# Optimization experiments

Hardware: AMD Instinct MI355X
Metric: run time of the kernel (lower is better)

## Reference

```python
import jax, jax.numpy as jnp
import numpy as np

N_HEAD = 16


def setup_inputs() -> dict:
    key = jax.random.key(0)
    ks = jax.random.split(key, 5)
    B, T, C = 2, 2048, 1024
    s = 1.0 / np.sqrt(C)
    inp = {
        "x": jax.random.normal(ks[0], (B, T, C), dtype=jnp.float32),
        "Wq": jax.random.normal(ks[1], (C, C), dtype=jnp.float32) * s,
        "bq": jnp.zeros((C,), dtype=jnp.float32),
        "Wk": jax.random.normal(ks[2], (C, C), dtype=jnp.float32) * s,
        "bk": jnp.zeros((C,), dtype=jnp.float32),
        "Wv": jax.random.normal(ks[3], (C, C), dtype=jnp.float32) * s,
        "bv": jnp.zeros((C,), dtype=jnp.float32),
        "Wp": jax.random.normal(ks[4], (C, C), dtype=jnp.float32) * s,
        "bp": jnp.zeros((C,), dtype=jnp.float32),
    }
    return inp


def reference(x, Wq, bq, Wk, bk, Wv, bv, Wp, bp):
    B, T, C = x.shape
    H = N_HEAD
    D = C // H
    # linear projections (torch Linear: x @ W.T + b)
    q = (x @ Wq.T + bq).reshape(B, T, H, D)
    k = (x @ Wk.T + bk).reshape(B, T, H, D)
    v = (x @ Wv.T + bv).reshape(B, T, H, D)
    # scaled dot-product attention (NO causal mask in original forward)
    att = jnp.einsum("bthd,bshd->bhts", q, k) * (1.0 / np.sqrt(D))
    att = jax.nn.softmax(att, axis=-1)
    y = jnp.einsum("bhts,bshd->bthd", att, v).reshape(B, T, C)
    # output projection (dropouts are identity at p=0 / eval)
    return y @ Wp.T + bp
```

## Files before the change

### kernel.cpp

```cpp
#include <hip/hip_runtime.h>
#include <hip/hip_bf16.h>

typedef __attribute__((ext_vector_type(4))) float f32x4;
typedef __attribute__((ext_vector_type(16))) float f32x16;
typedef __attribute__((ext_vector_type(8))) short bf16x8;
typedef __attribute__((ext_vector_type(2))) unsigned int u32x2;

#define T_SEQ 2048
#define C_DIM 1024
#define NH 16
#define DHD 64

__device__ __forceinline__ unsigned cvtpk_bf16(float lo, float hi) {
    unsigned r;
    asm("v_cvt_pk_bf16_f32 %0, %1, %2" : "=v"(r) : "v"(lo), "v"(hi));
    return r;
}

__device__ __forceinline__ float exp2_hw(float x) {
    float r;
    asm("v_exp_f32 %0, %1" : "=v"(r) : "v"(x));
    return r;
}

__device__ __forceinline__ void async_copy16(void* lds, const void* g) {
    __builtin_amdgcn_global_load_lds(
        (const __attribute__((address_space(1))) unsigned int*)(uintptr_t)g,
        (__attribute__((address_space(3))) unsigned int*)(unsigned int)(uintptr_t)lds,
        16, 0, 0);
}

__global__ __launch_bounds__(256) void cvt_all(const float* __restrict__ x,
                                               const float* __restrict__ Wq, const float* __restrict__ Wk,
                                               const float* __restrict__ Wv, const float* __restrict__ Wp,
                                               __hip_bfloat16* __restrict__ xb,
                                               __hip_bfloat16* __restrict__ wf,
                                               __hip_bfloat16* __restrict__ wpb) {
    int i = blockIdx.x * blockDim.x + threadIdx.x;
    const float* src; __hip_bfloat16* dst; int off;
    if (i < 1048576) { src = x; dst = xb; off = i; }
    else {
        int j = i - 1048576; int wi = j >> 18; off = j & 262143;
        switch (wi) {
            case 0:  src = Wq; dst = wf;           break;
            case 1:  src = Wk; dst = wf + 1048576; break;
            case 2:  src = Wv; dst = wf + 2097152; break;
            default: src = Wp; dst = wpb;          break;
        }
    }
    float4 v = *(const float4*)(src + (size_t)off * 4);
    union { __hip_bfloat16 h[4]; u32x2 u; } p;
    p.h[0] = __float2bfloat16(v.x); p.h[1] = __float2bfloat16(v.y);
    p.h[2] = __float2bfloat16(v.z); p.h[3] = __float2bfloat16(v.w);
    *(u32x2*)(dst + (size_t)off * 4) = p.u;
}

__global__ __launch_bounds__(512) void gemm_qkv(const __hip_bfloat16* __restrict__ A,
                                                const __hip_bfloat16* __restrict__ Bw,
                                                const float* __restrict__ biasq,
                                                const float* __restrict__ biask,
                                                const float* __restrict__ biasv,
                                                __hip_bfloat16* __restrict__ oq,
                                                __hip_bfloat16* __restrict__ okk,
                                                __hip_bfloat16* __restrict__ ovt) {
    __shared__ __align__(16) char lds[131072];

    const int xcd = (int)blockIdx.x & 7, loc = (int)blockIdx.x >> 3;
    const int mloc = loc / 6, nloc = loc - mloc * 6;
    const int m0 = ((xcd & 3) * 4 + mloc) * 256;
    const int n0 = ((xcd >> 2) * 6 + nloc) * 256;

    const int tid = threadIdx.x;
    const int w = tid >> 6, l = tid & 63;
    const int wr = w >> 2, wc = w & 3;
    const int lg = l >> 4, lr = l & 15;

    const int sr0 = tid >> 3;
    const int sc0 = (tid & 7) * 16;
    const int gc0 = sc0 ^ ((sr0 & 7) << 4);
    const size_t goff = (size_t)sr0 * 2048 + gc0;

    const char* Ag = (const char*)A + (size_t)m0 * 2048;
    const char* Bg = (const char*)Bw + (size_t)n0 * 2048;

    auto STAGE_A = [&](int buf, int half, int kt) {
        const char* g = Ag + (size_t)(half * 128) * 2048 + kt * 128 + goff;
        char* d = lds + (buf * 2 + half) * 16384 + w * 1024;
        async_copy16(d, g);
        async_copy16(d + 8192, g + (size_t)64 * 2048);
    };
    auto STAGE_B = [&](int buf, int half, int kt) {
        const char* g = Bg + (size_t)(half * 128) * 2048 + kt * 128 + goff;
        char* d = lds + 65536 + (buf * 2 + half) * 16384 + w * 1024;
        async_copy16(d, g);
        async_copy16(d + 8192, g + (size_t)64 * 2048);
    };

    const int sw = (lr & 7) << 4;
    auto LDA = [&](bf16x8* af, int buf, int mq) {
        const char* base = lds + (buf * 2 + wr) * 16384;
        #pragma unroll
        for (int m = 0; m < 4; m++) {
            const int r = (mq * 4 + m) * 16 + lr;
            #pragma unroll
            for (int kk = 0; kk < 2; kk++)
                af[m * 2 + kk] = *(const bf16x8*)(base + r * 128 + ((kk * 64 + lg * 16) ^ sw));
        }
    };
    auto LDB = [&](bf16x8* bfv, int buf, int nq) {
        const char* base = lds + 65536 + (buf * 2 + (wc >> 1)) * 16384;
        #pragma unroll
        for (int n = 0; n < 2; n++) {
            const int r = (wc & 1) * 64 + (nq * 2 + n) * 16 + lr;
            #pragma unroll
            for (int kk = 0; kk < 2; kk++)
                bfv[n * 2 + kk] = *(const bf16x8*)(base + r * 128 + ((kk * 64 + lg * 16) ^ sw));
        }
    };

    f32x4 acc[8][4] = {};
    auto MF = [&](const bf16x8* af, const bf16x8* bfv, int mq, int nq) {
        #pragma unroll
        for (int m = 0; m < 4; m++)
            #pragma unroll
            for (int n = 0; n < 2; n++)
                #pragma unroll
                for (int kk = 0; kk < 2; kk++)
                    acc[mq * 4 + m][nq * 2 + n] = __builtin_amdgcn_mfma_f32_16x16x32_bf16(
                        af[m * 2 + kk], bfv[n * 2 + kk], acc[mq * 4 + m][nq * 2 + n], 0, 0, 0);
    };

#define PH_OPEN()  __builtin_amdgcn_sched_barrier(0); \
                   __builtin_amdgcn_s_barrier(); \
                   asm volatile("s_waitcnt lgkmcnt(0)" ::: "memory"); \
                   __builtin_amdgcn_sched_barrier(0); \
                   __builtin_amdgcn_s_setprio(1);
#define PH_CLOSE() __builtin_amdgcn_s_setprio(0); \
                   __builtin_amdgcn_sched_barrier(0); \
                   __builtin_amdgcn_s_barrier();
#define PH_CLOSE_VM() __builtin_amdgcn_s_setprio(0); \
                   asm volatile("s_waitcnt vmcnt(6)" ::: "memory"); \
                   __builtin_amdgcn_sched_barrier(0); \
                   __builtin_amdgcn_s_barrier();

    bf16x8 af[8], bf0[4], bf1[4];

    STAGE_B(0, 0, 0); STAGE_B(0, 1, 0); STAGE_A(0, 0, 0); STAGE_A(0, 1, 0);
    STAGE_B(1, 0, 1); STAGE_B(1, 1, 1); STAGE_A(1, 0, 1);
    asm volatile("s_waitcnt vmcnt(6)" ::: "memory");
    __builtin_amdgcn_sched_barrier(0);
    __builtin_amdgcn_s_barrier();

    for (int it = 0; it < 8; ++it) {
        const int t1 = 2 * it + 1;
        const int c2 = (2 * it + 2 < 16) ? 2 * it + 2 : 14;
        const int c3 = (2 * it + 3 < 16) ? 2 * it + 3 : 15;
        const int b2 = c2 & 1, b3 = c3 & 1;

        LDA(af, 0, 0); LDB(bf0, 0, 0);
        STAGE_A(1, 1, t1);
        PH_OPEN(); MF(af, bf0, 0, 0); PH_CLOSE();
        LDB(bf1, 0, 1);
        PH_OPEN(); MF(af, bf1, 0, 1); PH_CLOSE();
        LDA(af, 0, 1);
        STAGE_B(b2, 0, c2);
        PH_OPEN(); MF(af, bf1, 1, 1); PH_CLOSE();
        STAGE_B(b2, 1, c2); STAGE_A(b2, 0, c2);
        PH_OPEN(); MF(af, bf0, 1, 0); PH_CLOSE_VM();

        LDA(af, 1, 0); LDB(bf0, 1, 0);
        STAGE_A(b2, 1, c2);
        PH_OPEN(); MF(af, bf0, 0, 0); PH_CLOSE();
        LDB(bf1, 1, 1);
        PH_OPEN(); MF(af, bf1, 0, 1); PH_CLOSE();
        LDA(af, 1, 1);
        STAGE_B(b3, 0, c3);
        PH_OPEN(); MF(af, bf1, 1, 1); PH_CLOSE();
        STAGE_B(b3, 1, c3); STAGE_A(b3, 0, c3);
        PH_OPEN(); MF(af, bf0, 1, 0); PH_CLOSE_VM();
    }
#undef PH_OPEN
#undef PH_CLOSE
#undef PH_CLOSE_VM

    const int proj = n0 >> 10;
    if (proj < 2) {
        const float* bias = (proj == 0) ? biasq : biask;
        const float bsc = (proj == 0) ? 0.125f * 1.4426950408889634f : 1.0f;
        __hip_bfloat16* dst = (proj == 0) ? oq : okk;
        #pragma unroll
        for (int m = 0; m < 8; m++)
            #pragma unroll
            for (int n = 0; n < 4; n++)
                #pragma unroll
                for (int rr = 0; rr < 4; rr++) {
                    int row = m0 + wr * 128 + m * 16 + lg * 4 + rr;
                    int col = n0 + wc * 64 + n * 16 + lr;
                    int colL = col & (C_DIM - 1);
                    float val = (acc[m][n][rr] + bias[colL]) * bsc;
                    int b = row >> 11, t = row & 2047, hh = colL >> 6, dd = colL & 63;
                    dst[(((size_t)(b * NH + hh)) * T_SEQ + t) * DHD + dd] = __float2bfloat16(val);
                }
    } else {
        #pragma unroll
        for (int m = 0; m < 8; m++) {
            const int rowb = m0 + wr * 128 + m * 16 + lg * 4;
            const int b = rowb >> 11, t0 = rowb & 2047;
            #pragma unroll
            for (int n = 0; n < 4; n++) {
                int col = n0 + wc * 64 + n * 16 + lr;
                int colL = col & (C_DIM - 1);
                int hh = colL >> 6, dd = colL & 63;
                float bv = biasv[colL];
                union { __hip_bfloat16 h[4]; u32x2 u; } p;
                #pragma unroll
                for (int rr = 0; rr < 4; rr++)
                    p.h[rr] = __float2bfloat16(acc[m][n][rr] + bv);
                *(u32x2*)&ovt[(((size_t)(b * NH + hh)) * DHD + dd) * T_SEQ + t0] = p.u;
            }
        }
    }
}

__global__ __launch_bounds__(256) void gemm_proj(const __hip_bfloat16* __restrict__ A,
                                                 const __hip_bfloat16* __restrict__ Bw,
                                                 const float* __restrict__ biasp,
                                                 float* __restrict__ outf) {
    __shared__ __align__(16) char As[128 * 128];
    __shared__ __align__(16) char Bs[128 * 128];

    const int nwg = gridDim.x;
    const int cpx = nwg >> 3;
    const int wg = ((int)blockIdx.x & 7) * cpx + ((int)blockIdx.x >> 3);
    const int m0 = (wg & 31) * 128;
    const int n0 = (wg >> 5) * 128;

    const int tid = threadIdx.x;
    const int w = tid >> 6, l = tid & 63;
    const int wr = w >> 1, wc = w & 1;
    const int lg = l >> 4, lr = l & 15;

    const char* Ag = (const char*)A + (size_t)m0 * 2048;
    const char* Bg = (const char*)Bw + (size_t)n0 * 2048;
    const int lrow = l >> 3;
    const int scol = (l & 7) * 16;

    f32x4 acc[4][4] = {};

    for (int kt = 0; kt < 16; ++kt) {
        __syncthreads();
        #pragma unroll
        for (int i = 0; i < 4; i++) {
            const int rb = w * 32 + i * 8;
            const size_t go = (size_t)(rb + lrow) * 2048 + (size_t)kt * 128 + scol;
            async_copy16(&As[rb * 128], Ag + go);
            async_copy16(&Bs[rb * 128], Bg + go);
        }
        __syncthreads();
        #pragma unroll
        for (int kk = 0; kk < 2; kk++) {
            bf16x8 af[4], bfr[4];
            #pragma unroll
            for (int m = 0; m < 4; m++)
                af[m] = *(const bf16x8*)(&As[(wr * 64 + m * 16 + lr) * 128 + kk * 64 + lg * 16]);
            #pragma unroll
            for (int n = 0; n < 4; n++)
                bfr[n] = *(const bf16x8*)(&Bs[(wc * 64 + n * 16 + lr) * 128 + kk * 64 + lg * 16]);
            #pragma unroll
            for (int m = 0; m < 4; m++)
                #pragma unroll
                for (int n = 0; n < 4; n++)
                    acc[m][n] = __builtin_amdgcn_mfma_f32_16x16x32_bf16(af[m], bfr[n], acc[m][n], 0, 0, 0);
        }
    }

    #pragma unroll
    for (int m = 0; m < 4; m++)
        #pragma unroll
        for (int n = 0; n < 4; n++)
            #pragma unroll
            for (int r = 0; r < 4; r++) {
                int row = m0 + wr * 64 + m * 16 + lg * 4 + r;
                int col = n0 + wc * 64 + n * 16 + lr;
                outf[(size_t)row * C_DIM + col] = acc[m][n][r] + biasp[col];
            }
}

__global__ __launch_bounds__(256) void attn5(const __hip_bfloat16* __restrict__ Q,
                                             const __hip_bfloat16* __restrict__ K,
                                             const __hip_bfloat16* __restrict__ Vt,
                                             __hip_bfloat16* __restrict__ Y) {
    const int bid = blockIdx.x;
    const int xcd = bid & 7, slot = bid >> 3;
    const int head = xcd * 4 + (slot & 3);
    const int qblk = slot >> 2;

    const int tid = threadIdx.x;
    const int w = tid >> 6, l = tid & 63;
    const int lq = l & 31, hi = l >> 5;
    const int q0 = qblk * 128 + w * 32;

    __shared__ __align__(16) char Ks[3][8192];
    __shared__ float bc[4][32];

    const char* Kb = (const char*)(K + (size_t)head * T_SEQ * DHD);
    const char* Vb = (const char*)(Vt + (size_t)head * DHD * T_SEQ);

    bf16x8 qf[4];
    {
        const char* qrow = (const char*)(Q + ((size_t)head * T_SEQ + q0 + lq) * DHD);
        #pragma unroll
        for (int t = 0; t < 4; t++) qf[t] = *(const bf16x8*)(qrow + t * 32 + hi * 16);
    }

    f32x16 yacc[2] = {};
    float ls0 = 0.f, ls1 = 0.f, ls2 = 0.f, ls3 = 0.f;

    const int o0 = (2 * w) * 1024 + l * 16;
    const int o1 = o0 + 1024;
    const int r0 = o0 >> 7, c0b = o0 & 127;
    const int r1 = o1 >> 7, c1b = o1 & 127;
    const int wads0 = r0 * 128 + (c0b ^ ((r0 & 7) << 4));
    const int wads1 = r1 * 128 + (c1b ^ ((r1 & 7) << 4));

    float4 kreg0, kreg1;
    auto stage_load = [&](int tile) {
        const char* kb2 = Kb + (size_t)tile * 8192;
        kreg0 = *(const float4*)(kb2 + o0);
        kreg1 = *(const float4*)(kb2 + o1);
    };
    auto stage_write = [&](int buf) {
        *(float4*)(&Ks[buf][wads0]) = kreg0;
        *(float4*)(&Ks[buf][wads1]) = kreg1;
    };

    auto qk = [&](int buf, f32x16& s0h, f32x16& s1h) {
        s0h = f32x16{}; s1h = f32x16{};
        const char* base0 = Ks[buf] + (0 * 32 + lq) * 128;
        const char* base1 = Ks[buf] + (1 * 32 + lq) * 128;
        const int sw0 = (lq & 7) << 4;
        #pragma unroll
        for (int t = 0; t < 4; t++) {
            bf16x8 kf0 = *(const bf16x8*)(base0 + ((t * 32 + hi * 16) ^ sw0));
            s0h = __builtin_amdgcn_mfma_f32_32x32x16_bf16(kf0, qf[t], s0h, 0, 0, 0);
        }
        #pragma unroll
        for (int t = 0; t < 4; t++) {
            bf16x8 kf1 = *(const bf16x8*)(base1 + ((t * 32 + hi * 16) ^ sw0));
            s1h = __builtin_amdgcn_mfma_f32_32x32x16_bf16(kf1, qf[t], s1h, 0, 0, 0);
        }
    };

    auto sm_exp = [&](f32x16& a, f32x16& b) {
        #pragma unroll
        for (int r = 0; r < 16; r += 4) {
            a[r + 0] = exp2_hw(a[r + 0]); a[r + 1] = exp2_hw(a[r + 1]);
            a[r + 2] = exp2_hw(a[r + 2]); a[r + 3] = exp2_hw(a[r + 3]);
            b[r + 0] = exp2_hw(b[r + 0]); b[r + 1] = exp2_hw(b[r + 1]);
            b[r + 2] = exp2_hw(b[r + 2]); b[r + 3] = exp2_hw(b[r + 3]);
            ls0 += a[r + 0] + b[r + 0];
            ls1 += a[r + 1] + b[r + 1];
            ls2 += a[r + 2] + b[r + 2];
            ls3 += a[r + 3] + b[r + 3];
        }
    };

    auto pv = [&](int tile, const f32x16& a, const f32x16& b) {
        bf16x8 vf[8];
        const char* vb = Vb + (size_t)tile * 128;
        #pragma unroll
        for (int t = 0; t < 4; t++)
            #pragma unroll
            for (int dh = 0; dh < 2; dh++)
                vf[t * 2 + dh] = *(const bf16x8*)(vb + (size_t)(dh * 32 + lq) * (T_SEQ * 2) + t * 32 + hi * 16);
        unsigned pw0[8], pw1[8];
        #pragma unroll
        for (int M = 0; M < 4; M++) {
            const int u = M * 4;
            pw0[M] = cvtpk_bf16(a[u + 0], a[u + 1]);
            pw1[M] = cvtpk_bf16(a[u + 2], a[u + 3]);
            pw0[M + 4] = cvtpk_bf16(b[u + 0], b[u + 1]);
            pw1[M + 4] = cvtpk_bf16(b[u + 2], b[u + 3]);
        }
        #pragma unroll
        for (int t = 0; t < 4; t++) {
            u32x2 s0p = __builtin_amdgcn_permlane32_swap(pw0[2 * t], pw0[2 * t + 1], false, false);
            u32x2 s1p = __builtin_amdgcn_permlane32_swap(pw1[2 * t], pw1[2 * t + 1], false, false);
            union { unsigned u[4]; bf16x8 v; } af;
            af.u[0] = s0p.x; af.u[1] = s1p.x; af.u[2] = s0p.y; af.u[3] = s1p.y;
            #pragma unroll
            for (int dh = 0; dh < 2; dh++)
                yacc[dh] = __builtin_amdgcn_mfma_f32_32x32x16_bf16(af.v, vf[t * 2 + dh], yacc[dh], 0, 0, 0);
        }
    };

    f32x16 sA0, sA1, sB0, sB1;
    stage_load(0); stage_write(0);
    stage_load(1); stage_write(1);
    stage_load(2);
    __syncthreads();
    qk(0, sA0, sA1);

    for (int t = 0; t < 32; t += 2) {
        qk((t + 1) % 3, sB0, sB1);
        if (t + 2 < 32) {
            asm volatile("s_waitcnt vmcnt(0)" ::: "memory");
            stage_write((t + 2) % 3);
            if (t + 3 < 32) stage_load(t + 3);
        }
        sm_exp(sA0, sA1);
        pv(t, sA0, sA1);
        asm volatile("s_waitcnt lgkmcnt(0)" ::: "memory");
        __builtin_amdgcn_s_barrier();
        __builtin_amdgcn_sched_barrier(0);

        const int t1 = t + 1;
        if (t1 + 1 < 32) qk((t1 + 1) % 3, sA0, sA1);
        if (t1 + 2 < 32) {
            asm volatile("s_waitcnt vmcnt(0)" ::: "memory");
            stage_write((t1 + 2) % 3);
            if (t1 + 3 < 32) stage_load(t1 + 3);
        }
        sm_exp(sB0, sB1);
        pv(t1, sB0, sB1);
        asm volatile("s_waitcnt lgkmcnt(0)" ::: "memory");
        __builtin_amdgcn_s_barrier();
        __builtin_amdgcn_sched_barrier(0);
    }

    float lsum = (ls0 + ls1) + (ls2 + ls3);
    lsum += __shfl_xor(lsum, 32);
    float inv = 1.0f / lsum;
    if (hi == 0) bc[w][lq] = inv;
    asm volatile("s_waitcnt lgkmcnt(0)" ::: "memory");
    __builtin_amdgcn_sched_barrier(0);

    const int b = head >> 4, h16 = head & 15;
    const size_t rowbase = (size_t)b * T_SEQ + q0;
    #pragma unroll
    for (int r = 0; r < 16; r++) {
        const int crow = (r & 3) + 8 * (r >> 2) + 4 * hi;
        const float iv = bc[w][crow];
        const size_t row = rowbase + crow;
        Y[row * C_DIM + h16 * DHD + lq]      = __float2bfloat16(yacc[0][r] * iv);
        Y[row * C_DIM + h16 * DHD + 32 + lq] = __float2bfloat16(yacc[1][r] * iv);
    }
}

extern "C" void kernel_launch(void* const* d_in, const int* in_sizes, int n_in,
                              void* d_out, int out_size, void* d_ws, size_t ws_size,
                              hipStream_t stream) {
    (void)in_sizes; (void)n_in; (void)out_size; (void)ws_size;
    const float* x  = (const float*)d_in[0];
    const float* Wq = (const float*)d_in[1];
    const float* bq = (const float*)d_in[2];
    const float* Wk = (const float*)d_in[3];
    const float* bk = (const float*)d_in[4];
    const float* Wv = (const float*)d_in[5];
    const float* bv = (const float*)d_in[6];
    const float* Wp = (const float*)d_in[7];
    const float* bp = (const float*)d_in[8];
    float* out = (float*)d_out;

    char* ws = (char*)d_ws;
    const size_t MC = (size_t)4096 * C_DIM;
    const size_t CC = (size_t)C_DIM * C_DIM;
    __hip_bfloat16* xb  = (__hip_bfloat16*)ws;  ws += MC * 2;
    __hip_bfloat16* wf  = (__hip_bfloat16*)ws;  ws += 3 * CC * 2;
    __hip_bfloat16* wpb = (__hip_bfloat16*)ws;  ws += CC * 2;
    __hip_bfloat16* qb  = (__hip_bfloat16*)ws;  ws += MC * 2;
    __hip_bfloat16* kb  = (__hip_bfloat16*)ws;  ws += MC * 2;
    __hip_bfloat16* vtb = (__hip_bfloat16*)ws;  ws += MC * 2;
    __hip_bfloat16* yb  = (__hip_bfloat16*)ws;  ws += MC * 2;

    cvt_all<<<8192, 256, 0, stream>>>(x, Wq, Wk, Wv, Wp, xb, wf, wpb);

    gemm_qkv<<<192, 512, 0, stream>>>(xb, wf, bq, bk, bv, qb, kb, vtb);

    attn5<<<512, 256, 0, stream>>>(qb, kb, vtb, yb);

    gemm_proj<<<256, 256, 0, stream>>>(yb, wpb, bp, out);
}
```

Measured before the change: 138.7 us.

## Stage V tiles through shared memory triple buffer and raise MFMA priority

V^T tiles are now staged through a swizzled triple-buffered LDS ring, the same way K is, so PV reads come from shared memory instead of each wave fetching directly from global memory. This removes redundant per-wave global V loads and makes them coalesced, prefetched stage loads. The QK and PV MFMA sections are also wrapped in s_setprio to favour the matrix work. In exchange, LDS use doubles, which may reduce occupancy, and more LDS traffic is added.

```diff
diff --git a/kernel.cpp b/kernel.cpp
--- a/kernel.cpp
+++ b/kernel.cpp
@@ -286,7 +286,7 @@
             }
 }
 
-__global__ __launch_bounds__(256) void attn5(const __hip_bfloat16* __restrict__ Q,
+__global__ __launch_bounds__(256) void attn8(const __hip_bfloat16* __restrict__ Q,
                                              const __hip_bfloat16* __restrict__ K,
                                              const __hip_bfloat16* __restrict__ Vt,
                                              __hip_bfloat16* __restrict__ Y) {
@@ -301,6 +301,7 @@
     const int q0 = qblk * 128 + w * 32;
 
     __shared__ __align__(16) char Ks[3][8192];
+    __shared__ __align__(16) char Vs[3][8192];
     __shared__ float bc[4][32];
 
     const char* Kb = (const char*)(K + (size_t)head * T_SEQ * DHD);
@@ -322,23 +323,30 @@
     const int r1 = o1 >> 7, c1b = o1 & 127;
     const int wads0 = r0 * 128 + (c0b ^ ((r0 & 7) << 4));
     const int wads1 = r1 * 128 + (c1b ^ ((r1 & 7) << 4));
-
-    float4 kreg0, kreg1;
+    const char* vsrc0 = Vb + (size_t)r0 * (T_SEQ * 2) + c0b;
+    const char* vsrc1 = Vb + (size_t)r1 * (T_SEQ * 2) + c1b;
+
+    float4 kreg0, kreg1, vreg0, vreg1;
     auto stage_load = [&](int tile) {
         const char* kb2 = Kb + (size_t)tile * 8192;
         kreg0 = *(const float4*)(kb2 + o0);
         kreg1 = *(const float4*)(kb2 + o1);
+        vreg0 = *(const float4*)(vsrc0 + (size_t)tile * 128);
+        vreg1 = *(const float4*)(vsrc1 + (size_t)tile * 128);
     };
     auto stage_write = [&](int buf) {
         *(float4*)(&Ks[buf][wads0]) = kreg0;
         *(float4*)(&Ks[buf][wads1]) = kreg1;
+        *(float4*)(&Vs[buf][wads0]) = vreg0;
+        *(float4*)(&Vs[buf][wads1]) = vreg1;
     };
 
     auto qk = [&](int buf, f32x16& s0h, f32x16& s1h) {
         s0h = f32x16{}; s1h = f32x16{};
-        const char* base0 = Ks[buf] + (0 * 32 + lq) * 128;
-        const char* base1 = Ks[buf] + (1 * 32 + lq) * 128;
+        const char* base0 = Ks[buf] + lq * 128;
+        const char* base1 = Ks[buf] + (32 + lq) * 128;
         const int sw0 = (lq & 7) << 4;
+        __builtin_amdgcn_s_setprio(1);
         #pragma unroll
         for (int t = 0; t < 4; t++) {
             bf16x8 kf0 = *(const bf16x8*)(base0 + ((t * 32 + hi * 16) ^ sw0));
@@ -349,6 +357,7 @@
             bf16x8 kf1 = *(const bf16x8*)(base1 + ((t * 32 + hi * 16) ^ sw0));
             s1h = __builtin_amdgcn_mfma_f32_32x32x16_bf16(kf1, qf[t], s1h, 0, 0, 0);
         }
+        __builtin_amdgcn_s_setprio(0);
     };
 
     auto sm_exp = [&](f32x16& a, f32x16& b) {
@@ -365,14 +374,7 @@
         }
     };
 
-    auto pv = [&](int tile, const f32x16& a, const f32x16& b) {
-        bf16x8 vf[8];
-        const char* vb = Vb + (size_t)tile * 128;
-        #pragma unroll
-        for (int t = 0; t < 4; t++)
-            #pragma unroll
-            for (int dh = 0; dh < 2; dh++)
-                vf[t * 2 + dh] = *(const bf16x8*)(vb + (size_t)(dh * 32 + lq) * (T_SEQ * 2) + t * 32 + hi * 16);
+    auto pv = [&](int buf, const f32x16& a, const f32x16& b) {
         unsigned pw0[8], pw1[8];
         #pragma unroll
         for (int M = 0; M < 4; M++) {
@@ -382,6 +384,7 @@
             pw0[M + 4] = cvtpk_bf16(b[u + 0], b[u + 1]);
             pw1[M + 4] = cvtpk_bf16(b[u + 2], b[u + 3]);
         }
+        __builtin_amdgcn_s_setprio(1);
         #pragma unroll
         for (int t = 0; t < 4; t++) {
             u32x2 s0p = __builtin_amdgcn_permlane32_swap(pw0[2 * t], pw0[2 * t + 1], false, false);
@@ -389,9 +392,13 @@
             union { unsigned u[4]; bf16x8 v; } af;
             af.u[0] = s0p.x; af.u[1] = s1p.x; af.u[2] = s0p.y; af.u[3] = s1p.y;
             #pragma unroll
-            for (int dh = 0; dh < 2; dh++)
-                yacc[dh] = __builtin_amdgcn_mfma_f32_32x32x16_bf16(af.v, vf[t * 2 + dh], yacc[dh], 0, 0, 0);
-        }
+            for (int dh = 0; dh < 2; dh++) {
+                const int row = dh * 32 + lq;
+                bf16x8 vf = *(const bf16x8*)(&Vs[buf][row * 128 + ((t * 32 + hi * 16) ^ ((row & 7) << 4))]);
+                yacc[dh] = __builtin_amdgcn_mfma_f32_32x32x16_bf16(af.v, vf, yacc[dh], 0, 0, 0);
+            }
+        }
+        __builtin_amdgcn_s_setprio(0);
     };
 
     f32x16 sA0, sA1, sB0, sB1;
@@ -409,7 +416,7 @@
             if (t + 3 < 32) stage_load(t + 3);
         }
         sm_exp(sA0, sA1);
-        pv(t, sA0, sA1);
+        pv(t % 3, sA0, sA1);
         asm volatile("s_waitcnt lgkmcnt(0)" ::: "memory");
         __builtin_amdgcn_s_barrier();
         __builtin_amdgcn_sched_barrier(0);
@@ -422,7 +429,7 @@
             if (t1 + 3 < 32) stage_load(t1 + 3);
         }
         sm_exp(sB0, sB1);
-        pv(t1, sB0, sB1);
+        pv(t1 % 3, sB0, sB1);
         asm volatile("s_waitcnt lgkmcnt(0)" ::: "memory");
         __builtin_amdgcn_s_barrier();
         __builtin_amdgcn_sched_barrier(0);
@@ -477,7 +484,7 @@
 
     gemm_qkv<<<192, 512, 0, stream>>>(xb, wf, bq, bk, bv, qb, kb, vtb);
 
-    attn5<<<512, 256, 0, stream>>>(qb, kb, vtb, yb);
+    attn8<<<512, 256, 0, stream>>>(qb, kb, vtb, yb);
 
     gemm_proj<<<256, 256, 0, stream>>>(yb, wpb, bp, out);
 }
```

After: 120.2 us. 1.15x faster.
